# Kernel tuning notes

Hardware: AMD Instinct MI355X
Metric: run time of the kernel (lower is better)

The kernel has to match this reference:

```python
import jax, jax.numpy as jnp
import numpy as np

N_EMBD = 768
HEAD_SIZE = 64

def setup_inputs() -> dict:
    key = jax.random.key(0)
    k1, k2, k3, k4 = jax.random.split(key, 4)
    B, T = 8, 2048
    x = jax.random.normal(k1, (B, T, N_EMBD), dtype=jnp.float32)
    s = 1.0 / np.sqrt(N_EMBD)
    Wk = jax.random.normal(k2, (N_EMBD, HEAD_SIZE), dtype=jnp.float32) * s
    Wq = jax.random.normal(k3, (N_EMBD, HEAD_SIZE), dtype=jnp.float32) * s
    Wv = jax.random.normal(k4, (N_EMBD, HEAD_SIZE), dtype=jnp.float32) * s
    return {"x": x, "Wk": Wk, "Wq": Wq, "Wv": Wv}

def reference(x, Wk, Wq, Wv):
    # x: [B, T, C]; projections: [B, T, H]
    B, T, C = x.shape
    k = jnp.einsum('btc,ch->bth', x, Wk)
    q = jnp.einsum('btc,ch->bth', x, Wq)
    v = jnp.einsum('btc,ch->bth', x, Wv)
    # scores [B, T, T], scaled by head_size^-0.5
    wei = jnp.einsum('bth,bsh->bts', q, k) * (HEAD_SIZE ** -0.5)
    causal = jnp.tril(jnp.ones((T, T), dtype=bool))
    wei = jnp.where(causal, wei, -jnp.inf)
    wei = jax.nn.softmax(wei, axis=-1)
    # dropout omitted (eval mode / deterministic reference)
    out = jnp.einsum('bts,bsh->bth', wei, v)
    return out
```

## Files before the change

kernel.cpp:

```cpp
#include <hip/hip_runtime.h>

#define B_ 8
#define T_ 2048
#define C_ 768
#define H_ 64
#define QT_ (T_ / 64)
#define NCH_ 8

typedef __bf16 bf16x8 __attribute__((ext_vector_type(8)));
typedef unsigned short ushort8 __attribute__((ext_vector_type(8)));
typedef float f32x4 __attribute__((ext_vector_type(4)));
typedef float f32x16 __attribute__((ext_vector_type(16)));

typedef __attribute__((address_space(1))) const void g_void;
typedef __attribute__((address_space(3))) void lds_void;

static __device__ __forceinline__ unsigned short f32_to_bf16(float f) {
  unsigned int u = __float_as_uint(f);
  u += 0x7FFFu + ((u >> 16) & 1u);
  return (unsigned short)(u >> 16);
}

static __device__ __forceinline__ float bf16_to_f32(unsigned short u) {
  return __uint_as_float(((unsigned int)u) << 16);
}

static __device__ __forceinline__ unsigned int cvtpk_bf16(float a, float b) {
  unsigned int r;
  asm("v_cvt_pk_bf16_f32 %0, %1, %2" : "=v"(r) : "v"(a), "v"(b));
  return r;
}

static __device__ __forceinline__ f32x4 mfma16(ushort8 a, ushort8 b, f32x4 c) {
  return __builtin_amdgcn_mfma_f32_16x16x32_bf16(
      __builtin_bit_cast(bf16x8, a), __builtin_bit_cast(bf16x8, b), c, 0, 0, 0);
}

static __device__ __forceinline__ f32x16 mfma32(ushort8 a, ushort8 b, f32x16 c) {
  return __builtin_amdgcn_mfma_f32_32x32x16_bf16(
      __builtin_bit_cast(bf16x8, a), __builtin_bit_cast(bf16x8, b), c, 0, 0, 0);
}

template <int BASE>
static __device__ __forceinline__ ushort8 packA(const f32x16& p) {
  unsigned int a1 = cvtpk_bf16(p[BASE + 0], p[BASE + 1]);
  unsigned int a2 = cvtpk_bf16(p[BASE + 2], p[BASE + 3]);
  unsigned int a3 = cvtpk_bf16(p[BASE + 4], p[BASE + 5]);
  unsigned int a4 = cvtpk_bf16(p[BASE + 6], p[BASE + 7]);
  asm("v_permlane32_swap_b32 %0, %1" : "+v"(a1), "+v"(a3));
  asm("v_permlane32_swap_b32 %0, %1" : "+v"(a2), "+v"(a4));
  uint4 w = {a1, a2, a3, a4};
  return __builtin_bit_cast(ushort8, w);
}

__global__ void prep_w_kernel(const float* __restrict__ Wk, const float* __restrict__ Wq,
                              const float* __restrict__ Wv, unsigned short* __restrict__ Wt) {
  int g = blockIdx.x * 256 + threadIdx.x;
  if (g >= 24 * 768) return;
  int ks = g / 768, s = g - ks * 768;
  int n = s >> 2, perm = s & 3;
  int k8 = perm ^ (n & 3) ^ ((n >> 2) & 3);
  int p = n >> 6, col = n & 63;
  const float* W = (p == 0) ? Wk : (p == 1) ? Wq : Wv;
  float sc = (p == 1) ? 0.125f * 1.44269504088896f : 1.0f;
  int kbase = ks * 32 + k8 * 8;
  ushort8 v;
#pragma unroll
  for (int e = 0; e < 8; ++e) v[e] = f32_to_bf16(W[(kbase + e) * 64 + col] * sc);
  *(ushort8*)(Wt + (size_t)g * 8) = v;
}

__global__ __launch_bounds__(512) void proj_kernel(
    const float* __restrict__ x, const unsigned short* __restrict__ Wt,
    unsigned short* __restrict__ Qf, unsigned short* __restrict__ Kf,
    unsigned short* __restrict__ Vf) {
  __shared__ unsigned short Wl[2][6144];
  __shared__ unsigned short Xl[2][1024];
  const int tid = threadIdx.x;
  const int wave = tid >> 6, lane = tid & 63;
  const int lo = lane & 15, hi = lane >> 4;
  const int rg = wave & 1, ch3 = wave >> 1;
  const int row0 = blockIdx.x * 32;

  f32x4 acc[3];
#pragma unroll
  for (int t = 0; t < 3; ++t) acc[t] = (f32x4){0.f, 0.f, 0.f, 0.f};

  const int xr = (tid & 127) >> 2;
  const int xk8 = tid & 3;
  const int xslot = xr * 4 + (xk8 ^ (xr & 3) ^ ((xr >> 2) & 3));
  const float* xsrc = x + (size_t)(row0 + xr) * C_ + xk8 * 8;

  const int arow = rg * 16 + lo;
  const int aaddr = (arow * 4 + (hi ^ (arow & 3) ^ ((arow >> 2) & 3))) * 8;

  auto wstage = [&](int buf, int ks) {
    const unsigned short* base = Wt + (size_t)ks * 6144 + lane * 8;
    for (int is = wave; is < 12; is += 8)
      __builtin_amdgcn_global_load_lds((g_void*)(base + is * 512),
          (lds_void*)(&Wl[buf][is * 512]), 16, 0, 0);
  };

  float4 xa0 = {}, xa1 = {}, xb0 = {}, xb1 = {};

  wstage(0, 0);
  if (tid < 128) {
    xa0 = *(const float4*)(xsrc);
    xa1 = *(const float4*)(xsrc + 4);
  }

  for (int ks = 0; ks < 24; ++ks) {
    const int cur = ks & 1;
    asm volatile("s_waitcnt vmcnt(0)" ::: "memory");
    __syncthreads();
    if (ks + 1 < 24) {
      wstage(cur ^ 1, ks + 1);
      if (tid < 128) {
        xb0 = *(const float4*)(xsrc + (ks + 1) * 32);
        xb1 = *(const float4*)(xsrc + (ks + 1) * 32 + 4);
      }
    }
    if (tid < 128) {
      unsigned int dd[4];
      dd[0] = cvtpk_bf16(xa0.x, xa0.y);
      dd[1] = cvtpk_bf16(xa0.z, xa0.w);
      dd[2] = cvtpk_bf16(xa1.x, xa1.y);
      dd[3] = cvtpk_bf16(xa1.z, xa1.w);
      *(uint4*)(&Xl[cur][xslot * 8]) = *(uint4*)dd;
    }
    __syncthreads();
    ushort8 af = *(const ushort8*)(&Xl[cur][aaddr]);
#pragma unroll
    for (int t = 0; t < 3; ++t) {
      const int n = ch3 * 48 + t * 16 + lo;
      const int baddr = (n * 4 + (hi ^ (n & 3) ^ ((n >> 2) & 3))) * 8;
      ushort8 bfr = *(const ushort8*)(&Wl[cur][baddr]);
      acc[t] = mfma16(af, bfr, acc[t]);
    }
    xa0 = xb0; xa1 = xb1;
  }

#pragma unroll
  for (int t = 0; t < 3; ++t) {
    const int n = ch3 * 48 + t * 16 + lo;
    const int p = n >> 6, d = n & 63;
#pragma unroll
    for (int r = 0; r < 4; ++r) {
      const int rgl = row0 + rg * 16 + hi * 4 + r;
      const int b = rgl >> 11;
      const int tt = rgl & (T_ - 1);
      unsigned short val = f32_to_bf16(acc[t][r]);
      if (p == 2) {
        const size_t addr = ((((size_t)b * 128 + (tt >> 4)) * 2 + (d >> 5)) * 64 +
                             ((tt >> 3) & 1) * 32 + (d & 31)) * 8 + (tt & 7);
        Vf[addr] = val;
      } else {
        const size_t addr = ((((size_t)b * 64 + (tt >> 5)) * 4 + (d >> 4)) * 64 +
                             ((d >> 3) & 1) * 32 + (tt & 31)) * 8 + (d & 7);
        if (p == 0) Kf[addr] = val; else Qf[addr] = val;
      }
    }
  }
}

__global__ __launch_bounds__(128) void attn_part_kernel(
    const unsigned short* __restrict__ Qf, const unsigned short* __restrict__ Kf,
    const unsigned short* __restrict__ Vf, unsigned short* __restrict__ Opb,
    float* __restrict__ Ml) {
  const int id = blockIdx.x;
  const int b = id & 7;
  const int r2 = id >> 3;
  const int qt = r2 & 31;
  const int ch = r2 >> 5;
  const int t0 = ch * 4;
  if (t0 > qt) return;
  const int t1 = min(qt, t0 + 3);

  const int tid = threadIdx.x;
  const int wave = tid >> 6;
  const int lane = tid & 63;
  const int il = lane & 31;
  const int h = lane >> 5;
  const int i0w = qt * 64 + wave * 32;

  const unsigned short* qbase = Qf + ((((size_t)b * 64 + (qt * 2 + wave)) * 4) << 9) + lane * 8;
  const unsigned short* kbase = Kf + (((size_t)b * 64) << 11) + lane * 8;
  const unsigned short* vbase = Vf + (((size_t)b * 128) << 10) + lane * 8;

  ushort8 qf[4];
#pragma unroll
  for (int dc = 0; dc < 4; ++dc) qf[dc] = *(const ushort8*)(qbase + (dc << 9));

  f32x16 o0 = {}, o1 = {};
  float m = -1e30f, lsum = 0.f;

  for (int jt = t0; jt <= t1; ++jt) {
    const int j0 = jt * 64;
    const size_t jg = (size_t)(jt * 2);

    ushort8 kf0[4], kf1[4];
#pragma unroll
    for (int dc = 0; dc < 4; ++dc) {
      kf0[dc] = *(const ushort8*)(kbase + (jg << 11) + (dc << 9));
      kf1[dc] = *(const ushort8*)(kbase + ((jg + 1) << 11) + (dc << 9));
    }
    ushort8 vf0[4], vf1[4];
#pragma unroll
    for (int c = 0; c < 4; ++c) {
      const size_t jc = (size_t)(jt * 4 + c);
      vf0[c] = *(const ushort8*)(vbase + (jc << 10));
      vf1[c] = *(const ushort8*)(vbase + (jc << 10) + (1 << 9));
    }

    f32x16 s0 = {}, s1 = {};
    __builtin_amdgcn_s_setprio(1);
#pragma unroll
    for (int dc = 0; dc < 4; ++dc) {
      s0 = mfma32(kf0[dc], qf[dc], s0);
      s1 = mfma32(kf1[dc], qf[dc], s1);
    }
    __builtin_amdgcn_s_setprio(0);

    if (jt == qt) {
      const int ig = i0w + il;
#pragma unroll
      for (int r = 0; r < 16; ++r) {
        const int jl = j0 + (r & 3) + 8 * (r >> 2) + 4 * h;
        if (jl > ig) s0[r] = -1e30f;
        if (jl + 32 > ig) s1[r] = -1e30f;
      }
    }

    float mx[8];
#pragma unroll
    for (int r = 0; r < 8; ++r) mx[r] = fmaxf(fmaxf(s0[r], s0[r + 8]), fmaxf(s1[r], s1[r + 8]));
#pragma unroll
    for (int d = 4; d >= 1; d >>= 1)
#pragma unroll
      for (int r = 0; r < d; ++r) mx[r] = fmaxf(mx[r], mx[r + d]);
    float tm = fmaxf(mx[0], __shfl_xor(mx[0], 32));
    float scl = 1.0f;
    if (!__all(tm <= m + 8.0f)) {
      const float mnew = fmaxf(m, tm);
      scl = exp2f(m - mnew);
      m = mnew;
      o0 *= scl;
      o1 *= scl;
    }
    float sa = 0.f, sb = 0.f, sc2 = 0.f, sd = 0.f;
#pragma unroll
    for (int r = 0; r < 16; r += 4) {
      s0[r] = exp2f(s0[r] - m);     sa += s0[r];
      s0[r + 1] = exp2f(s0[r + 1] - m); sb += s0[r + 1];
      s0[r + 2] = exp2f(s0[r + 2] - m); sc2 += s0[r + 2];
      s0[r + 3] = exp2f(s0[r + 3] - m); sd += s0[r + 3];
    }
#pragma unroll
    for (int r = 0; r < 16; r += 4) {
      s1[r] = exp2f(s1[r] - m);     sa += s1[r];
      s1[r + 1] = exp2f(s1[r + 1] - m); sb += s1[r + 1];
      s1[r + 2] = exp2f(s1[r + 2] - m); sc2 += s1[r + 2];
      s1[r + 3] = exp2f(s1[r + 3] - m); sd += s1[r + 3];
    }
    float ts = (sa + sb) + (sc2 + sd);
    ts += __shfl_xor(ts, 32);
    lsum = lsum * scl + ts;

    __builtin_amdgcn_s_setprio(1);
#pragma unroll
    for (int c = 0; c < 4; ++c) {
      ushort8 pa = (c == 0) ? packA<0>(s0) : (c == 1) ? packA<8>(s0)
                 : (c == 2) ? packA<0>(s1) : packA<8>(s1);
      o0 = mfma32(vf0[c], pa, o0);
      o1 = mfma32(vf1[c], pa, o1);
    }
    __builtin_amdgcn_s_setprio(0);
  }

  const size_t pb = (size_t)(b * QT_ + qt) * NCH_ + ch;
  unsigned short* op = Opb + pb * 4096 + (size_t)(wave * 32 + il) * 64;
#pragma unroll
  for (int g = 0; g < 4; ++g) {
    unsigned int w0[2], w1[2];
    w0[0] = cvtpk_bf16(o0[4 * g + 0], o0[4 * g + 1]);
    w0[1] = cvtpk_bf16(o0[4 * g + 2], o0[4 * g + 3]);
    w1[0] = cvtpk_bf16(o1[4 * g + 0], o1[4 * g + 1]);
    w1[1] = cvtpk_bf16(o1[4 * g + 2], o1[4 * g + 3]);
    *(uint2*)(op + 8 * g + 4 * h) = *(uint2*)w0;
    *(uint2*)(op + 32 + 8 * g + 4 * h) = *(uint2*)w1;
  }
  if (h == 0) {
    float* ml = Ml + pb * 128;
    ml[wave * 32 + il] = m;
    ml[64 + wave * 32 + il] = lsum;
  }
}

__global__ __launch_bounds__(256) void attn_comb_kernel(
    const unsigned short* __restrict__ Opb, const float* __restrict__ Ml,
    float* __restrict__ out) {
  const int id = blockIdx.x;
  const int b = id & 7;
  const int qt = id >> 3;
  const int nc = (qt >> 2) + 1;
  const int row = threadIdx.x >> 2;
  const int c0 = (threadIdx.x & 3) * 16;
  const size_t pbase = (size_t)(b * QT_ + qt) * NCH_;

  float m_g = -1e30f;
  for (int c = 0; c < nc; ++c) m_g = fmaxf(m_g, Ml[(pbase + c) * 128 + row]);
  float l_g = 0.f;
  for (int c = 0; c < nc; ++c)
    l_g += Ml[(pbase + c) * 128 + 64 + row] * exp2f(Ml[(pbase + c) * 128 + row] - m_g);
  const float inv = 1.0f / l_g;

  f32x4 a0 = {0,0,0,0}, a1 = {0,0,0,0}, a2 = {0,0,0,0}, a3 = {0,0,0,0};
  for (int c = 0; c < nc; ++c) {
    const float wc = exp2f(Ml[(pbase + c) * 128 + row] - m_g);
    const unsigned short* op = Opb + (pbase + c) * 4096 + row * 64 + c0;
    ushort8 u0 = *(const ushort8*)(op);
    ushort8 u1 = *(const ushort8*)(op + 8);
    a0 += (f32x4){bf16_to_f32(u0[0]), bf16_to_f32(u0[1]), bf16_to_f32(u0[2]), bf16_to_f32(u0[3])} * wc;
    a1 += (f32x4){bf16_to_f32(u0[4]), bf16_to_f32(u0[5]), bf16_to_f32(u0[6]), bf16_to_f32(u0[7])} * wc;
    a2 += (f32x4){bf16_to_f32(u1[0]), bf16_to_f32(u1[1]), bf16_to_f32(u1[2]), bf16_to_f32(u1[3])} * wc;
    a3 += (f32x4){bf16_to_f32(u1[4]), bf16_to_f32(u1[5]), bf16_to_f32(u1[6]), bf16_to_f32(u1[7])} * wc;
  }
  float* o = out + ((size_t)b * T_ + qt * 64 + row) * 64 + c0;
  *(f32x4*)(o) = a0 * inv;
  *(f32x4*)(o + 4) = a1 * inv;
  *(f32x4*)(o + 8) = a2 * inv;
  *(f32x4*)(o + 12) = a3 * inv;
}

extern "C" void kernel_launch(void* const* d_in, const int* in_sizes, int n_in,
                              void* d_out, int out_size, void* d_ws, size_t ws_size,
                              hipStream_t stream) {
  const float* x = (const float*)d_in[0];
  const float* Wk = (const float*)d_in[1];
  const float* Wq = (const float*)d_in[2];
  const float* Wv = (const float*)d_in[3];
  float* out = (float*)d_out;

  char* ws = (char*)d_ws;
  unsigned short* Qf = (unsigned short*)(ws);
  unsigned short* Kf = (unsigned short*)(ws + (2u << 20));
  unsigned short* Vf = (unsigned short*)(ws + (4u << 20));
  unsigned short* Wt = (unsigned short*)(ws + (6u << 20));
  unsigned short* Opb = (unsigned short*)(ws + (8u << 20));
  float* Ml = (float*)(ws + (24u << 20));

  prep_w_kernel<<<dim3(72), dim3(256), 0, stream>>>(Wk, Wq, Wv, Wt);
  proj_kernel<<<dim3((B_ * T_) / 32), dim3(512), 0, stream>>>(x, Wt, Qf, Kf, Vf);
  attn_part_kernel<<<dim3(QT_ * B_ * NCH_), dim3(128), 0, stream>>>(Qf, Kf, Vf, Opb, Ml);
  attn_comb_kernel<<<dim3(QT_ * B_), dim3(256), 0, stream>>>(Opb, Ml, out);
}
```

Before: 54.61 us.

## Fuse split-KV combine into attention kernel via last-block atomic counter

Removes the separate combine kernel launch. Each partial-attention block increments a per-(batch, query-tile) counter after a threadfence, and the last block to finish merges all chunk partials into the final output. The counters are zeroed in the weight-prep kernel. This saves one launch and its tail, but adds atomics and fences, and the combine work now runs on a single 128-thread block per tile, covering two rows per thread.

New measurement: 157.0 us. +187.5%, slower.

```diff
diff --git a/kernel.cpp b/kernel.cpp
--- a/kernel.cpp
+++ b/kernel.cpp
@@ -54,8 +54,10 @@
 }
 
 __global__ void prep_w_kernel(const float* __restrict__ Wk, const float* __restrict__ Wq,
-                              const float* __restrict__ Wv, unsigned short* __restrict__ Wt) {
+                              const float* __restrict__ Wv, unsigned short* __restrict__ Wt,
+                              int* __restrict__ cnt) {
   int g = blockIdx.x * 256 + threadIdx.x;
+  if (g < B_ * QT_) cnt[g] = 0;
   if (g >= 24 * 768) return;
   int ks = g / 768, s = g - ks * 768;
   int n = s >> 2, perm = s & 3;
@@ -166,7 +168,7 @@
 __global__ __launch_bounds__(128) void attn_part_kernel(
     const unsigned short* __restrict__ Qf, const unsigned short* __restrict__ Kf,
     const unsigned short* __restrict__ Vf, unsigned short* __restrict__ Opb,
-    float* __restrict__ Ml) {
+    float* __restrict__ Ml, int* __restrict__ cnt, float* __restrict__ out) {
   const int id = blockIdx.x;
   const int b = id & 7;
   const int r2 = id >> 3;
@@ -175,6 +177,8 @@
   const int t0 = ch * 4;
   if (t0 > qt) return;
   const int t1 = min(qt, t0 + 3);
+
+  __shared__ int s_last;
 
   const int tid = threadIdx.x;
   const int wave = tid >> 6;
@@ -294,42 +298,46 @@
     ml[wave * 32 + il] = m;
     ml[64 + wave * 32 + il] = lsum;
   }
-}
-
-__global__ __launch_bounds__(256) void attn_comb_kernel(
-    const unsigned short* __restrict__ Opb, const float* __restrict__ Ml,
-    float* __restrict__ out) {
-  const int id = blockIdx.x;
-  const int b = id & 7;
-  const int qt = id >> 3;
+
   const int nc = (qt >> 2) + 1;
-  const int row = threadIdx.x >> 2;
-  const int c0 = (threadIdx.x & 3) * 16;
+  __threadfence();
+  if (tid == 0) {
+    int prev = atomicAdd(&cnt[b * QT_ + qt], 1);
+    s_last = (prev == nc - 1);
+  }
+  __syncthreads();
+  if (!s_last) return;
+  __threadfence();
+
   const size_t pbase = (size_t)(b * QT_ + qt) * NCH_;
-
-  float m_g = -1e30f;
-  for (int c = 0; c < nc; ++c) m_g = fmaxf(m_g, Ml[(pbase + c) * 128 + row]);
-  float l_g = 0.f;
-  for (int c = 0; c < nc; ++c)
-    l_g += Ml[(pbase + c) * 128 + 64 + row] * exp2f(Ml[(pbase + c) * 128 + row] - m_g);
-  const float inv = 1.0f / l_g;
-
-  f32x4 a0 = {0,0,0,0}, a1 = {0,0,0,0}, a2 = {0,0,0,0}, a3 = {0,0,0,0};
-  for (int c = 0; c < nc; ++c) {
-    const float wc = exp2f(Ml[(pbase + c) * 128 + row] - m_g);
-    const unsigned short* op = Opb + (pbase + c) * 4096 + row * 64 + c0;
-    ushort8 u0 = *(const ushort8*)(op);
-    ushort8 u1 = *(const ushort8*)(op + 8);
-    a0 += (f32x4){bf16_to_f32(u0[0]), bf16_to_f32(u0[1]), bf16_to_f32(u0[2]), bf16_to_f32(u0[3])} * wc;
-    a1 += (f32x4){bf16_to_f32(u0[4]), bf16_to_f32(u0[5]), bf16_to_f32(u0[6]), bf16_to_f32(u0[7])} * wc;
-    a2 += (f32x4){bf16_to_f32(u1[0]), bf16_to_f32(u1[1]), bf16_to_f32(u1[2]), bf16_to_f32(u1[3])} * wc;
-    a3 += (f32x4){bf16_to_f32(u1[4]), bf16_to_f32(u1[5]), bf16_to_f32(u1[6]), bf16_to_f32(u1[7])} * wc;
-  }
-  float* o = out + ((size_t)b * T_ + qt * 64 + row) * 64 + c0;
-  *(f32x4*)(o) = a0 * inv;
-  *(f32x4*)(o + 4) = a1 * inv;
-  *(f32x4*)(o + 8) = a2 * inv;
-  *(f32x4*)(o + 12) = a3 * inv;
+#pragma unroll
+  for (int it = 0; it < 2; ++it) {
+    const int wid = tid + it * 128;
+    const int row = wid >> 2;
+    const int c0 = (wid & 3) * 16;
+    float m_g = -1e30f;
+    for (int c = 0; c < nc; ++c) m_g = fmaxf(m_g, Ml[(pbase + c) * 128 + row]);
+    float l_g = 0.f;
+    for (int c = 0; c < nc; ++c)
+      l_g += Ml[(pbase + c) * 128 + 64 + row] * exp2f(Ml[(pbase + c) * 128 + row] - m_g);
+    const float inv = 1.0f / l_g;
+    f32x4 a0 = {0,0,0,0}, a1 = {0,0,0,0}, a2 = {0,0,0,0}, a3 = {0,0,0,0};
+    for (int c = 0; c < nc; ++c) {
+      const float wc = exp2f(Ml[(pbase + c) * 128 + row] - m_g);
+      const unsigned short* op2 = Opb + (pbase + c) * 4096 + row * 64 + c0;
+      ushort8 u0 = *(const ushort8*)(op2);
+      ushort8 u1 = *(const ushort8*)(op2 + 8);
+      a0 += (f32x4){bf16_to_f32(u0[0]), bf16_to_f32(u0[1]), bf16_to_f32(u0[2]), bf16_to_f32(u0[3])} * wc;
+      a1 += (f32x4){bf16_to_f32(u0[4]), bf16_to_f32(u0[5]), bf16_to_f32(u0[6]), bf16_to_f32(u0[7])} * wc;
+      a2 += (f32x4){bf16_to_f32(u1[0]), bf16_to_f32(u1[1]), bf16_to_f32(u1[2]), bf16_to_f32(u1[3])} * wc;
+      a3 += (f32x4){bf16_to_f32(u1[4]), bf16_to_f32(u1[5]), bf16_to_f32(u1[6]), bf16_to_f32(u1[7])} * wc;
+    }
+    float* o = out + ((size_t)b * T_ + qt * 64 + row) * 64 + c0;
+    *(f32x4*)(o) = a0 * inv;
+    *(f32x4*)(o + 4) = a1 * inv;
+    *(f32x4*)(o + 8) = a2 * inv;
+    *(f32x4*)(o + 12) = a3 * inv;
+  }
 }
 
 extern "C" void kernel_launch(void* const* d_in, const int* in_sizes, int n_in,
@@ -348,9 +356,9 @@
   unsigned short* Wt = (unsigned short*)(ws + (6u << 20));
   unsigned short* Opb = (unsigned short*)(ws + (8u << 20));
   float* Ml = (float*)(ws + (24u << 20));
-
-  prep_w_kernel<<<dim3(72), dim3(256), 0, stream>>>(Wk, Wq, Wv, Wt);
+  int* cnt = (int*)(ws + (25u << 20));
+
+  prep_w_kernel<<<dim3(72), dim3(256), 0, stream>>>(Wk, Wq, Wv, Wt, cnt);
   proj_kernel<<<dim3((B_ * T_) / 32), dim3(512), 0, stream>>>(x, Wt, Qf, Kf, Vf);
-  attn_part_kernel<<<dim3(QT_ * B_ * NCH_), dim3(128), 0, stream>>>(Qf, Kf, Vf, Opb, Ml);
-  attn_comb_kernel<<<dim3(QT_ * B_), dim3(256), 0, stream>>>(Opb, Ml, out);
-}
+  attn_part_kernel<<<dim3(QT_ * B_ * NCH_), dim3(128), 0, stream>>>(Qf, Kf, Vf, Opb, Ml, cnt, out);
+}
```

## Load projection operands directly into MFMA registers, dropping LDS staging

Applied to the files above, without the earlier changes.

The projection kernel no longer stages W and x through double-buffered shared memory with barriers. Instead, prep_w writes weights pre-arranged in MFMA fragment order, and each wave loads x fragments and weight fragments straight from global memory into registers. The block shrinks to 4 waves, with each wave computing 6 output tiles. This removes LDS traffic and __syncthreads stalls, but x rows are now read by both wave halves, weights are re-read per wave through cache, and there is no explicit prefetch to hide latency.

Result: slower. 60.99 us (+11.7%).

```diff
diff --git a/kernel.cpp b/kernel.cpp
--- a/kernel.cpp
+++ b/kernel.cpp
@@ -11,9 +11,6 @@
 typedef unsigned short ushort8 __attribute__((ext_vector_type(8)));
 typedef float f32x4 __attribute__((ext_vector_type(4)));
 typedef float f32x16 __attribute__((ext_vector_type(16)));
-
-typedef __attribute__((address_space(1))) const void g_void;
-typedef __attribute__((address_space(3))) void lds_void;
 
 static __device__ __forceinline__ unsigned short f32_to_bf16(float f) {
   unsigned int u = __float_as_uint(f);
@@ -54,95 +51,61 @@
 }
 
 __global__ void prep_w_kernel(const float* __restrict__ Wk, const float* __restrict__ Wq,
-                              const float* __restrict__ Wv, unsigned short* __restrict__ Wt) {
+                              const float* __restrict__ Wv, unsigned short* __restrict__ Wf) {
   int g = blockIdx.x * 256 + threadIdx.x;
-  if (g >= 24 * 768) return;
-  int ks = g / 768, s = g - ks * 768;
-  int n = s >> 2, perm = s & 3;
-  int k8 = perm ^ (n & 3) ^ ((n >> 2) & 3);
+  if (g >= 24 * 12 * 64) return;
+  int ks = g / 768;
+  int rem = g - ks * 768;
+  int tile = rem >> 6, lane = rem & 63;
+  int lo = lane & 15, hi = lane >> 4;
+  int n = tile * 16 + lo;
   int p = n >> 6, col = n & 63;
   const float* W = (p == 0) ? Wk : (p == 1) ? Wq : Wv;
   float sc = (p == 1) ? 0.125f * 1.44269504088896f : 1.0f;
-  int kbase = ks * 32 + k8 * 8;
   ushort8 v;
 #pragma unroll
-  for (int e = 0; e < 8; ++e) v[e] = f32_to_bf16(W[(kbase + e) * 64 + col] * sc);
-  *(ushort8*)(Wt + (size_t)g * 8) = v;
-}
-
-__global__ __launch_bounds__(512) void proj_kernel(
-    const float* __restrict__ x, const unsigned short* __restrict__ Wt,
+  for (int e = 0; e < 8; ++e)
+    v[e] = f32_to_bf16(W[(ks * 32 + hi * 8 + e) * 64 + col] * sc);
+  *(ushort8*)(Wf + (size_t)g * 8) = v;
+}
+
+__global__ __launch_bounds__(256) void proj_kernel(
+    const float* __restrict__ x, const unsigned short* __restrict__ Wf,
     unsigned short* __restrict__ Qf, unsigned short* __restrict__ Kf,
     unsigned short* __restrict__ Vf) {
-  __shared__ unsigned short Wl[2][6144];
-  __shared__ unsigned short Xl[2][1024];
   const int tid = threadIdx.x;
   const int wave = tid >> 6, lane = tid & 63;
   const int lo = lane & 15, hi = lane >> 4;
-  const int rg = wave & 1, ch3 = wave >> 1;
+  const int rg = wave & 1, half = wave >> 1;
   const int row0 = blockIdx.x * 32;
 
-  f32x4 acc[3];
-#pragma unroll
-  for (int t = 0; t < 3; ++t) acc[t] = (f32x4){0.f, 0.f, 0.f, 0.f};
-
-  const int xr = (tid & 127) >> 2;
-  const int xk8 = tid & 3;
-  const int xslot = xr * 4 + (xk8 ^ (xr & 3) ^ ((xr >> 2) & 3));
-  const float* xsrc = x + (size_t)(row0 + xr) * C_ + xk8 * 8;
-
-  const int arow = rg * 16 + lo;
-  const int aaddr = (arow * 4 + (hi ^ (arow & 3) ^ ((arow >> 2) & 3))) * 8;
-
-  auto wstage = [&](int buf, int ks) {
-    const unsigned short* base = Wt + (size_t)ks * 6144 + lane * 8;
-    for (int is = wave; is < 12; is += 8)
-      __builtin_amdgcn_global_load_lds((g_void*)(base + is * 512),
-          (lds_void*)(&Wl[buf][is * 512]), 16, 0, 0);
-  };
-
-  float4 xa0 = {}, xa1 = {}, xb0 = {}, xb1 = {};
-
-  wstage(0, 0);
-  if (tid < 128) {
-    xa0 = *(const float4*)(xsrc);
-    xa1 = *(const float4*)(xsrc + 4);
-  }
-
+  f32x4 acc[6];
+#pragma unroll
+  for (int t = 0; t < 6; ++t) acc[t] = (f32x4){0.f, 0.f, 0.f, 0.f};
+
+  const float* xrow = x + (size_t)(row0 + rg * 16 + lo) * C_ + hi * 8;
+  const unsigned short* wb = Wf + (half * 6) * 512 + lane * 8;
+
+#pragma unroll 2
   for (int ks = 0; ks < 24; ++ks) {
-    const int cur = ks & 1;
-    asm volatile("s_waitcnt vmcnt(0)" ::: "memory");
-    __syncthreads();
-    if (ks + 1 < 24) {
-      wstage(cur ^ 1, ks + 1);
-      if (tid < 128) {
-        xb0 = *(const float4*)(xsrc + (ks + 1) * 32);
-        xb1 = *(const float4*)(xsrc + (ks + 1) * 32 + 4);
-      }
-    }
-    if (tid < 128) {
-      unsigned int dd[4];
-      dd[0] = cvtpk_bf16(xa0.x, xa0.y);
-      dd[1] = cvtpk_bf16(xa0.z, xa0.w);
-      dd[2] = cvtpk_bf16(xa1.x, xa1.y);
-      dd[3] = cvtpk_bf16(xa1.z, xa1.w);
-      *(uint4*)(&Xl[cur][xslot * 8]) = *(uint4*)dd;
-    }
-    __syncthreads();
-    ushort8 af = *(const ushort8*)(&Xl[cur][aaddr]);
-#pragma unroll
-    for (int t = 0; t < 3; ++t) {
-      const int n = ch3 * 48 + t * 16 + lo;
-      const int baddr = (n * 4 + (hi ^ (n & 3) ^ ((n >> 2) & 3))) * 8;
-      ushort8 bfr = *(const ushort8*)(&Wl[cur][baddr]);
+    float4 a0 = *(const float4*)(xrow + ks * 32);
+    float4 a1 = *(const float4*)(xrow + ks * 32 + 4);
+    unsigned int dd[4];
+    dd[0] = cvtpk_bf16(a0.x, a0.y);
+    dd[1] = cvtpk_bf16(a0.z, a0.w);
+    dd[2] = cvtpk_bf16(a1.x, a1.y);
+    dd[3] = cvtpk_bf16(a1.z, a1.w);
+    ushort8 af = __builtin_bit_cast(ushort8, *(uint4*)dd);
+#pragma unroll
+    for (int t = 0; t < 6; ++t) {
+      ushort8 bfr = *(const ushort8*)(wb + ks * 6144 + t * 512);
       acc[t] = mfma16(af, bfr, acc[t]);
     }
-    xa0 = xb0; xa1 = xb1;
-  }
-
-#pragma unroll
-  for (int t = 0; t < 3; ++t) {
-    const int n = ch3 * 48 + t * 16 + lo;
+  }
+
+#pragma unroll
+  for (int t = 0; t < 6; ++t) {
+    const int n = half * 96 + t * 16 + lo;
     const int p = n >> 6, d = n & 63;
 #pragma unroll
     for (int r = 0; r < 4; ++r) {
@@ -345,12 +308,12 @@
   unsigned short* Qf = (unsigned short*)(ws);
   unsigned short* Kf = (unsigned short*)(ws + (2u << 20));
   unsigned short* Vf = (unsigned short*)(ws + (4u << 20));
-  unsigned short* Wt = (unsigned short*)(ws + (6u << 20));
+  unsigned short* Wf = (unsigned short*)(ws + (6u << 20));
   unsigned short* Opb = (unsigned short*)(ws + (8u << 20));
   float* Ml = (float*)(ws + (24u << 20));
 
-  prep_w_kernel<<<dim3(72), dim3(256), 0, stream>>>(Wk, Wq, Wv, Wt);
-  proj_kernel<<<dim3((B_ * T_) / 32), dim3(512), 0, stream>>>(x, Wt, Qf, Kf, Vf);
+  prep_w_kernel<<<dim3(72), dim3(256), 0, stream>>>(Wk, Wq, Wv, Wf);
+  proj_kernel<<<dim3((B_ * T_) / 32), dim3(256), 0, stream>>>(x, Wf, Qf, Kf, Vf);
   attn_part_kernel<<<dim3(QT_ * B_ * NCH_), dim3(128), 0, stream>>>(Qf, Kf, Vf, Opb, Ml);
   attn_comb_kernel<<<dim3(QT_ * B_), dim3(256), 0, stream>>>(Opb, Ml, out);
 }
```
